# Kernel tuning notes

Hardware: AMD Instinct MI355X
Metric: run time of the kernel (lower is better)

## Reference

```python
import jax, jax.numpy as jnp
import numpy as np

N = 50000        # total nodes (disjoint batch of graphs)
E = 800000       # total edges
F_IN = 8         # node feature dim
S = 6            # edge feature dim
H = 20           # ECC kernel-network hidden size (hidden_states)
N_OUT = 20       # ECC output channels (n_out=hidden_states)
G = 32           # GCN channels
D1 = 16          # first dense
N_GRAPHS = 512   # graphs in batch


def setup_inputs() -> dict:
    key = jax.random.key(0)
    ks = jax.random.split(key, 24)
    r = lambda k, sh, s: jax.random.normal(k, sh, dtype=jnp.float32) * s
    return {
        "x": r(ks[0], (N, F_IN), 1.0),
        "e": r(ks[1], (E, S), 1.0),
        "edge_index": jax.random.randint(ks[2], (2, E), 0, N, dtype=jnp.int32),
        "seg": jnp.sort(jax.random.randint(ks[3], (N,), 0, N_GRAPHS, dtype=jnp.int32)),
        # ECC kernel network: S -> H -> H -> F_IN*N_OUT
        "ecc_w1": r(ks[4], (S, H), 0.4), "ecc_b1": jnp.zeros((H,), jnp.float32),
        "ecc_w2": r(ks[5], (H, H), 0.2), "ecc_b2": jnp.zeros((H,), jnp.float32),
        "ecc_w3": r(ks[6], (H, F_IN * N_OUT), 0.2), "ecc_b3": jnp.zeros((F_IN * N_OUT,), jnp.float32),
        "ecc_root": r(ks[7], (F_IN, N_OUT), 0.3), "ecc_b": jnp.zeros((N_OUT,), jnp.float32),
        "gcn1_w": r(ks[8], (N_OUT, G), 0.2), "gcn1_b": jnp.zeros((G,), jnp.float32),
        "gcn2_w": r(ks[9], (G, G), 0.2), "gcn2_b": jnp.zeros((G,), jnp.float32),
        "d1_w": r(ks[10], (G, D1), 0.2), "d1_b": jnp.zeros((D1,), jnp.float32),
        "d2_w": r(ks[11], (D1, 1), 0.2), "d2_b": jnp.zeros((1,), jnp.float32),
    }


def reference(x, e, edge_index, seg,
              ecc_w1, ecc_b1, ecc_w2, ecc_b2, ecc_w3, ecc_b3, ecc_root, ecc_b,
              gcn1_w, gcn1_b, gcn2_w, gcn2_b, d1_w, d1_b, d2_w, d2_b):
    row, col = edge_index[0], edge_index[1]  # message col -> row

    # --- ECCConv: per-edge MLP produces an [F_IN, N_OUT] filter per edge ---
    h = jax.nn.relu(e @ ecc_w1 + ecc_b1)
    h = jax.nn.relu(h @ ecc_w2 + ecc_b2)
    w_edge = (h @ ecc_w3 + ecc_b3).reshape(E, F_IN, N_OUT)   # [E, F_in, F_out]
    msg = jnp.einsum('ef,efo->eo', x[col], w_edge)            # per-edge message
    agg = jax.ops.segment_sum(msg, row, num_segments=N)
    x1 = jax.nn.relu(agg + x @ ecc_root + ecc_b)              # root + bias + relu

    # --- GCN normalization from the edge list (A + I, symmetric norm) ---
    deg = jax.ops.segment_sum(jnp.ones((E,), x.dtype), row, num_segments=N) + 1.0
    dinv = jax.lax.rsqrt(deg)
    edge_norm = (dinv[row] * dinv[col])[:, None]
    self_norm = (dinv * dinv)[:, None]

    def gcn(hin, W, b):
        hw = hin @ W
        nmsg = jax.ops.segment_sum(edge_norm * hw[col], row, num_segments=N)
        return jax.nn.relu(nmsg + self_norm * hw + b)

    x2 = gcn(x1, gcn1_w, gcn1_b)
    x3 = gcn(x2, gcn2_w, gcn2_b)

    # --- GlobalSumPool over graph ids, then MLP head ---
    pooled = jax.ops.segment_sum(x3, seg, num_segments=N_GRAPHS)  # [n_graphs, G]
    out = (pooled @ d1_w + d1_b) @ d2_w + d2_b                    # [n_graphs, 1]
    return out
```

## Files before the change

kernel.cpp:

```cpp
#include <hip/hip_runtime.h>

#define S_DIM   6
#define H_DIM   20
#define F_INN   8
#define N_OUTC  20
#define G_DIM   32
#define D1_DIM  16
#define NGRAPH  512

typedef short short8 __attribute__((ext_vector_type(8)));
typedef float floatx4 __attribute__((ext_vector_type(4)));

__device__ __forceinline__ unsigned short f2bf(float f) {
    unsigned u = __float_as_uint(f);
    return (unsigned short)((u + 0x8000u) >> 16);
}
__device__ __forceinline__ float bf2f(unsigned short s) {
    return __uint_as_float(((unsigned)s) << 16);
}

__global__ __launch_bounds__(256) void loc_kernel(
    const int* __restrict__ ei, int E, int* __restrict__ cnt,
    int* __restrict__ loc)
{
    int i = blockIdx.x * 256 + threadIdx.x;
    if (i >= E) return;
    loc[i] = atomicAdd(&cnt[ei[i]], 1);
}

__global__ __launch_bounds__(256) void scanA_kernel(
    const int* __restrict__ deg, int N, int* __restrict__ bsum)
{
    int i = blockIdx.x * 256 + threadIdx.x;
    int v = (i < N) ? deg[i] : 0;
#pragma unroll
    for (int d = 1; d < 64; d <<= 1) v += __shfl_down(v, d, 64);
    __shared__ int ws[4];
    int wid = threadIdx.x >> 6;
    if ((threadIdx.x & 63) == 0) ws[wid] = v;
    __syncthreads();
    if (threadIdx.x == 0) bsum[blockIdx.x] = ws[0] + ws[1] + ws[2] + ws[3];
}

__global__ __launch_bounds__(256) void scanC_kernel(
    const int* __restrict__ deg, int N, const int* __restrict__ bsum, int nbl,
    int E, int* __restrict__ rowptr, float* __restrict__ dinv)
{
    __shared__ int ws[4];
    __shared__ int sboff;
    int t = threadIdx.x;
    {
        int v = (t < nbl && t < blockIdx.x) ? bsum[t] : 0;
#pragma unroll
        for (int d = 1; d < 64; d <<= 1) v += __shfl_down(v, d, 64);
        int wid = t >> 6;
        if ((t & 63) == 0) ws[wid] = v;
        __syncthreads();
        if (t == 0) sboff = ws[0] + ws[1] + ws[2] + ws[3];
        __syncthreads();
    }

    int i = blockIdx.x * 256 + t;
    int d0 = (i < N) ? deg[i] : 0;
    int v = d0;
#pragma unroll
    for (int d = 1; d < 64; d <<= 1) {
        int u = __shfl_up(v, d, 64);
        if ((t & 63) >= d) v += u;
    }
    __shared__ int ws2[4];
    int wid = t >> 6;
    if ((t & 63) == 63) ws2[wid] = v;
    __syncthreads();
    int woff = 0;
    for (int w = 0; w < wid; ++w) woff += ws2[w];
    if (i < N) {
        rowptr[i] = sboff + woff + v - d0;
        dinv[i] = rsqrtf((float)d0 + 1.0f);
    }
    if (blockIdx.x == 0 && t == 0) rowptr[N] = E;
}

__global__ __launch_bounds__(256) void build_kernel(
    const int* __restrict__ ei, int E, const int* __restrict__ rowptr,
    const int* __restrict__ loc,
    int* __restrict__ eid_at_slot, int* __restrict__ col_sorted)
{
    int i = blockIdx.x * 256 + threadIdx.x;
    if (i >= E) return;
    int p = rowptr[ei[i]] + loc[i];
    eid_at_slot[p] = i;
    col_sorted[p] = ei[E + i];
}

__global__ __launch_bounds__(256) void ecc_mfma_kernel(
    const float* __restrict__ e, const float* __restrict__ x,
    const int* __restrict__ eid_at_slot, const int* __restrict__ col_sorted,
    const int* __restrict__ rowptr, int N, int E,
    const float* __restrict__ w1, const float* __restrict__ b1,
    const float* __restrict__ w2, const float* __restrict__ b2,
    const float* __restrict__ w3, const float* __restrict__ b3,
    float* __restrict__ agg)
{
    __shared__ char ubuf[256 * N_OUTC * 4];
    __shared__ unsigned short h2b[256][N_OUTC];
    __shared__ unsigned short xb[256][F_INN];
    __shared__ int rbounds[2];

    unsigned short* Bl = (unsigned short*)ubuf;
    float* lmsg = (float*)ubuf;

    int t = threadIdx.x;
    int j0 = blockIdx.x * 256;
    int jend = min(j0 + 256, E);
    int j = j0 + t;

    if (t < 2) {
        int s = (t == 0) ? j0 : (jend - 1);
        int lo = 0, hi = N - 1;
        while (lo < hi) {
            int m = (lo + hi + 1) >> 1;
            if (rowptr[m] <= s) lo = m; else hi = m - 1;
        }
        rbounds[t] = lo;
    }

    for (int idx = t; idx < 6144; idx += 256) {
        int jj   = idx & 7;
        int n    = (idx >> 3) & 15;
        int quad = (idx >> 7) & 3;
        int nt   = (idx >> 9) & 1;
        int s    = idx >> 10;
        int K = 32 * s + quad * 8 + jj;
        int o = n + 16 * nt;
        float v = 0.0f;
        if (o < N_OUTC) {
            if (K < 160)      v = w3[(K >> 3) * 160 + (K & 7) * N_OUTC + o];
            else if (K < 168) v = b3[(K - 160) * N_OUTC + o];
        }
        Bl[idx] = f2bf(v);
    }

    if (j < E) {
        int i = eid_at_slot[j];
        int c = col_sorted[j];

        float ef[S_DIM];
#pragma unroll
        for (int s = 0; s < S_DIM; ++s) ef[s] = e[(size_t)i * S_DIM + s];

        float h1[H_DIM];
#pragma unroll
        for (int jj = 0; jj < H_DIM; ++jj) {
            float a = b1[jj];
#pragma unroll
            for (int s = 0; s < S_DIM; ++s) a = fmaf(ef[s], w1[s * H_DIM + jj], a);
            h1[jj] = fmaxf(a, 0.0f);
        }

        float h2[H_DIM];
#pragma unroll
        for (int jj = 0; jj < H_DIM; ++jj) {
            float a = b2[jj];
#pragma unroll
            for (int k = 0; k < H_DIM; ++k) a = fmaf(h1[k], w2[k * H_DIM + jj], a);
            h2[jj] = fmaxf(a, 0.0f);
        }

        const float4* xp = (const float4*)&x[(size_t)c * F_INN];
        float4 xa = xp[0], xb4 = xp[1];
        float xf[F_INN] = {xa.x, xa.y, xa.z, xa.w, xb4.x, xb4.y, xb4.z, xb4.w};

#pragma unroll
        for (int o = 0; o < N_OUTC; ++o) h2b[t][o] = f2bf(h2[o]);
#pragma unroll
        for (int f = 0; f < F_INN; ++f) xb[t][f] = f2bf(xf[f]);
    } else {
#pragma unroll
        for (int o = 0; o < N_OUTC; ++o) h2b[t][o] = 0;
#pragma unroll
        for (int f = 0; f < F_INN; ++f) xb[t][f] = 0;
    }
    __syncthreads();

    int lane = t & 63;
    int quad = lane >> 4;
    int n = lane & 15;
    short8 Bf[12];
#pragma unroll
    for (int s = 0; s < 6; ++s)
#pragma unroll
        for (int nt = 0; nt < 2; ++nt)
            Bf[s * 2 + nt] = *(const short8*)&Bl[((((s * 2 + nt) * 4 + quad) * 16 + n) * 8)];
    __syncthreads();

    int w = t >> 6;
#pragma unroll
    for (int T = 0; T < 4; ++T) {
        int base = w * 64 + T * 16;
        int m = base + n;

        const short8 xv8 = *(const short8*)&xb[m][0];
        float xfl[F_INN];
#pragma unroll
        for (int jj = 0; jj < F_INN; ++jj) xfl[jj] = bf2f((unsigned short)xv8[jj]);

        floatx4 acc0 = {0.f, 0.f, 0.f, 0.f};
        floatx4 acc1 = {0.f, 0.f, 0.f, 0.f};
#pragma unroll
        for (int s = 0; s < 6; ++s) {
            short8 A = {0, 0, 0, 0, 0, 0, 0, 0};
            if (s < 5) {
                float h = bf2f(h2b[m][4 * s + quad]);
#pragma unroll
                for (int jj = 0; jj < F_INN; ++jj)
                    A[jj] = (short)f2bf(h * xfl[jj]);
            } else if (quad == 0) {
                A = xv8;
            }
            acc0 = __builtin_amdgcn_mfma_f32_16x16x32_bf16(A, Bf[s * 2 + 0], acc0, 0, 0, 0);
            acc1 = __builtin_amdgcn_mfma_f32_16x16x32_bf16(A, Bf[s * 2 + 1], acc1, 0, 0, 0);
        }

#pragma unroll
        for (int r = 0; r < 4; ++r) {
            int row = base + quad * 4 + r;
            lmsg[row * N_OUTC + n] = acc0[r];
            if (n < 4) lmsg[row * N_OUTC + 16 + n] = acc1[r];
        }
    }
    __syncthreads();

    int r0 = rbounds[0], r1 = rbounds[1];
    int work = (r1 - r0 + 1) * 5;
    for (int ww = t; ww < work; ww += 256) {
        int row = r0 + ww / 5;
        int q = ww - (ww / 5) * 5;
        int a0 = rowptr[row], a1 = rowptr[row + 1];
        int s0 = max(a0, j0), s1 = min(a1, jend);
        float4 acc = make_float4(0.f, 0.f, 0.f, 0.f);
        for (int s = s0; s < s1; ++s) {
            const float4 v = *(const float4*)&lmsg[(s - j0) * N_OUTC + q * 4];
            acc.x += v.x; acc.y += v.y; acc.z += v.z; acc.w += v.w;
        }
        float* dst = &agg[(size_t)row * N_OUTC + q * 4];
        if (a0 >= j0 && a1 <= jend) {
            *(float4*)dst = acc;
        } else {
            unsafeAtomicAdd(dst + 0, acc.x);
            unsafeAtomicAdd(dst + 1, acc.y);
            unsafeAtomicAdd(dst + 2, acc.z);
            unsafeAtomicAdd(dst + 3, acc.w);
        }
    }
}

__global__ __launch_bounds__(256) void node1_kernel(
    const float* __restrict__ agg, const float* __restrict__ x,
    const float* __restrict__ dinv, int N,
    const float* __restrict__ root, const float* __restrict__ eb,
    const float* __restrict__ g1w,
    float* __restrict__ hws1)
{
    int n = blockIdx.x * 256 + threadIdx.x;
    if (n >= N) return;

    const float4* xp = (const float4*)&x[(size_t)n * F_INN];
    float4 xa = xp[0], xb = xp[1];
    float xf[F_INN] = {xa.x, xa.y, xa.z, xa.w, xb.x, xb.y, xb.z, xb.w};

    float x1[N_OUTC];
#pragma unroll
    for (int o = 0; o < N_OUTC; ++o) {
        float a = agg[(size_t)n * N_OUTC + o] + eb[o];
#pragma unroll
        for (int f = 0; f < F_INN; ++f) a = fmaf(xf[f], root[f * N_OUTC + o], a);
        x1[o] = fmaxf(a, 0.0f);
    }

    float di = dinv[n];
    float4* hp = (float4*)&hws1[(size_t)n * G_DIM];
#pragma unroll
    for (int q = 0; q < G_DIM / 4; ++q) {
        float4 v;
        float* vv = &v.x;
#pragma unroll
        for (int u = 0; u < 4; ++u) {
            int g = q * 4 + u;
            float a = 0.0f;
#pragma unroll
            for (int o = 0; o < N_OUTC; ++o) a = fmaf(x1[o], g1w[o * G_DIM + g], a);
            vv[u] = a * di;
        }
        hp[q] = v;
    }
}

template<bool DO_MATMUL>
__global__ __launch_bounds__(256) void gcn_gather_kernel(
    const float* __restrict__ hws, const int* __restrict__ rowptr,
    const int* __restrict__ col_sorted, const float* __restrict__ dinv, int N,
    const float* __restrict__ bias, const float* __restrict__ w2,
    float* __restrict__ outbuf)
{
    __shared__ float x2s[32 * 33];
    __shared__ float w2s[G_DIM * G_DIM];

    int t = threadIdx.x;
    int nl = t >> 3;
    int q = t & 7;
    int n = blockIdx.x * 32 + nl;

    if (DO_MATMUL) {
        ((float4*)w2s)[t] = ((const float4*)w2)[t];
    }

    float4 xo = make_float4(0.f, 0.f, 0.f, 0.f);
    float di = 0.0f;
    if (n < N) {
        di = dinv[n];
        int j0 = rowptr[n], j1 = rowptr[n + 1];
        float4 s = *(const float4*)&hws[(size_t)n * G_DIM + q * 4];
        for (int j = j0; j < j1; ++j) {
            int c = col_sorted[j];
            float4 v = *(const float4*)&hws[(size_t)c * G_DIM + q * 4];
            s.x += v.x; s.y += v.y; s.z += v.z; s.w += v.w;
        }
        const float4 b4 = *(const float4*)&bias[q * 4];
        xo.x = fmaxf(fmaf(di, s.x, b4.x), 0.0f);
        xo.y = fmaxf(fmaf(di, s.y, b4.y), 0.0f);
        xo.z = fmaxf(fmaf(di, s.z, b4.z), 0.0f);
        xo.w = fmaxf(fmaf(di, s.w, b4.w), 0.0f);
    }

    if (DO_MATMUL) {
        x2s[nl * 33 + q * 4 + 0] = xo.x;
        x2s[nl * 33 + q * 4 + 1] = xo.y;
        x2s[nl * 33 + q * 4 + 2] = xo.z;
        x2s[nl * 33 + q * 4 + 3] = xo.w;
        __syncthreads();
        if (n < N) {
            float a0 = 0.f, a1 = 0.f, a2 = 0.f, a3 = 0.f;
            const float* xr = &x2s[nl * 33];
#pragma unroll
            for (int g = 0; g < G_DIM; ++g) {
                float xv = xr[g];
                a0 = fmaf(xv, w2s[g * G_DIM + q * 4 + 0], a0);
                a1 = fmaf(xv, w2s[g * G_DIM + q * 4 + 1], a1);
                a2 = fmaf(xv, w2s[g * G_DIM + q * 4 + 2], a2);
                a3 = fmaf(xv, w2s[g * G_DIM + q * 4 + 3], a3);
            }
            *(float4*)&outbuf[(size_t)n * G_DIM + q * 4] =
                make_float4(a0 * di, a1 * di, a2 * di, a3 * di);
        }
    } else {
        if (n < N)
            *(float4*)&outbuf[(size_t)n * G_DIM + q * 4] = xo;
    }
}

__global__ __launch_bounds__(256) void pool_head_kernel(
    const float* __restrict__ x3, const int* __restrict__ seg, int N,
    const float* __restrict__ d1w, const float* __restrict__ d1b,
    const float* __restrict__ d2w, const float* __restrict__ d2b,
    float* __restrict__ out)
{
    __shared__ float red[8][G_DIM];
    __shared__ float pvec[G_DIM];
    __shared__ int bounds[2];
    int g = blockIdx.x;
    int t = threadIdx.x;
    if (t < 2) {
        int target = g + t;
        int lo = 0, hi = N;
        while (lo < hi) {
            int m = (lo + hi) >> 1;
            if (seg[m] < target) lo = m + 1; else hi = m;
        }
        bounds[t] = lo;
    }
    __syncthreads();
    int n0 = bounds[0], n1 = bounds[1];
    int ch = t & (G_DIM - 1);
    int slice = t >> 5;
    float a = 0.0f;
    for (int n = n0 + slice; n < n1; n += 8)
        a += x3[(size_t)n * G_DIM + ch];
    red[slice][ch] = a;
    __syncthreads();
    if (slice == 0) {
        float s = red[0][ch];
#pragma unroll
        for (int k = 1; k < 8; ++k) s += red[k][ch];
        pvec[ch] = s;
    }
    __syncthreads();
    if (t < 64) {
        float acc = 0.0f;
        if (t < D1_DIM) {
            float tj = d1b[t];
#pragma unroll
            for (int gg = 0; gg < G_DIM; ++gg)
                tj = fmaf(pvec[gg], d1w[gg * D1_DIM + t], tj);
            acc = tj * d2w[t];
        }
#pragma unroll
        for (int d = 1; d < D1_DIM; d <<= 1) acc += __shfl_down(acc, d, 64);
        if (t == 0) out[g] = acc + d2b[0];
    }
}

extern "C" void kernel_launch(void* const* d_in, const int* in_sizes, int n_in,
                              void* d_out, int out_size, void* d_ws, size_t ws_size,
                              hipStream_t stream)
{
    const float* x    = (const float*)d_in[0];
    const float* e    = (const float*)d_in[1];
    const int*   ei   = (const int*)d_in[2];
    const int*   seg  = (const int*)d_in[3];
    const float* w1   = (const float*)d_in[4];
    const float* b1   = (const float*)d_in[5];
    const float* w2   = (const float*)d_in[6];
    const float* b2   = (const float*)d_in[7];
    const float* w3   = (const float*)d_in[8];
    const float* b3   = (const float*)d_in[9];
    const float* root = (const float*)d_in[10];
    const float* eb   = (const float*)d_in[11];
    const float* g1w  = (const float*)d_in[12];
    const float* g1b  = (const float*)d_in[13];
    const float* g2w  = (const float*)d_in[14];
    const float* g2b  = (const float*)d_in[15];
    const float* d1w  = (const float*)d_in[16];
    const float* d1b  = (const float*)d_in[17];
    const float* d2w  = (const float*)d_in[18];
    const float* d2b  = (const float*)d_in[19];

    const int N = in_sizes[3];
    const int E = in_sizes[1] / S_DIM;
    float* out = (float*)d_out;

    const int nbl = (N + 255) / 256;
    const int ebl = (E + 255) / 256;

    char* ws = (char*)d_ws;
    size_t off = 0;
    auto alloc = [&](size_t elems) -> char* {
        char* p = ws + off;
        off += ((elems * 4 + 15) & ~(size_t)15);
        return p;
    };
    int*   cnt        = (int*)  alloc(N);
    float* agg        = (float*)alloc((size_t)N * N_OUTC);
    size_t zero_bytes = off;
    int*   rowptr     = (int*)  alloc(N + 1);
    int*   bsum       = (int*)  alloc(nbl);
    float* dinv       = (float*)alloc(N);
    int*   loc        = (int*)  alloc(E);
    int*   eid_at_slot= (int*)  alloc(E);
    int*   col_sorted = (int*)  alloc(E);
    float* hws1       = (float*)alloc((size_t)N * G_DIM);
    float* hws2       = (float*)alloc((size_t)N * G_DIM);
    float* x3         = (float*)alloc((size_t)N * G_DIM);
    (void)ws_size;

    hipMemsetAsync(d_ws, 0, zero_bytes, stream);

    loc_kernel<<<ebl, 256, 0, stream>>>(ei, E, cnt, loc);
    scanA_kernel<<<nbl, 256, 0, stream>>>(cnt, N, bsum);
    scanC_kernel<<<nbl, 256, 0, stream>>>(cnt, N, bsum, nbl, E, rowptr, dinv);
    build_kernel<<<ebl, 256, 0, stream>>>(ei, E, rowptr, loc, eid_at_slot, col_sorted);
    ecc_mfma_kernel<<<ebl, 256, 0, stream>>>(e, x, eid_at_slot, col_sorted,
                                             rowptr, N, E,
                                             w1, b1, w2, b2, w3, b3, agg);
    node1_kernel<<<nbl, 256, 0, stream>>>(agg, x, dinv, N, root, eb, g1w, hws1);
    gcn_gather_kernel<true><<<(N + 31) / 32, 256, 0, stream>>>(
        hws1, rowptr, col_sorted, dinv, N, g1b, g2w, hws2);
    gcn_gather_kernel<false><<<(N + 31) / 32, 256, 0, stream>>>(
        hws2, rowptr, col_sorted, dinv, N, g2b, nullptr, x3);
    pool_head_kernel<<<NGRAPH, 256, 0, stream>>>(x3, seg, N, d1w, d1b, d2w, d2b, out);
}
```

Baseline: 306.8 us.

## Store GCN node features in bf16 and shrink ECC kernel shared memory

The intermediate node feature buffers (hws1, hws2, x3) move from fp32 to bf16, halving the bytes read in the random-neighbour gathers of both GCN layers and in pooling. The gather kernels now have each thread handle 8 channels with 16-byte loads, covering 64 nodes per block. Separately, the ECC kernel overlaps its message buffer with the B-fragment, h2 and x staging areas in one smaller shared array, keeping MFMA accumulators in registers until a barrier. This lowers LDS use for higher occupancy, at the cost of bf16 rounding error in the GCN activations and more register pressure.

```diff
diff --git a/kernel.cpp b/kernel.cpp
--- a/kernel.cpp
+++ b/kernel.cpp
@@ -102,13 +102,12 @@
     const float* __restrict__ w3, const float* __restrict__ b3,
     float* __restrict__ agg)
 {
-    __shared__ char ubuf[256 * N_OUTC * 4];
-    __shared__ unsigned short h2b[256][N_OUTC];
-    __shared__ unsigned short xb[256][F_INN];
+    __shared__ char smem[26624];
     __shared__ int rbounds[2];
-
-    unsigned short* Bl = (unsigned short*)ubuf;
-    float* lmsg = (float*)ubuf;
+    unsigned short* Bl = (unsigned short*)smem;
+    unsigned short (*h2b)[N_OUTC] = (unsigned short (*)[N_OUTC])(smem + 12288);
+    unsigned short (*xb)[F_INN]   = (unsigned short (*)[F_INN])(smem + 22528);
+    float* lmsg = (float*)smem;
 
     int t = threadIdx.x;
     int j0 = blockIdx.x * 256;
@@ -192,9 +191,9 @@
 #pragma unroll
         for (int nt = 0; nt < 2; ++nt)
             Bf[s * 2 + nt] = *(const short8*)&Bl[((((s * 2 + nt) * 4 + quad) * 16 + n) * 8)];
-    __syncthreads();
 
     int w = t >> 6;
+    floatx4 acc0s[4], acc1s[4];
 #pragma unroll
     for (int T = 0; T < 4; ++T) {
         int base = w * 64 + T * 16;
@@ -221,12 +220,19 @@
             acc0 = __builtin_amdgcn_mfma_f32_16x16x32_bf16(A, Bf[s * 2 + 0], acc0, 0, 0, 0);
             acc1 = __builtin_amdgcn_mfma_f32_16x16x32_bf16(A, Bf[s * 2 + 1], acc1, 0, 0, 0);
         }
-
+        acc0s[T] = acc0;
+        acc1s[T] = acc1;
+    }
+    __syncthreads();
+
+#pragma unroll
+    for (int T = 0; T < 4; ++T) {
+        int base = w * 64 + T * 16;
 #pragma unroll
         for (int r = 0; r < 4; ++r) {
             int row = base + quad * 4 + r;
-            lmsg[row * N_OUTC + n] = acc0[r];
-            if (n < 4) lmsg[row * N_OUTC + 16 + n] = acc1[r];
+            lmsg[row * N_OUTC + n] = acc0s[T][r];
+            if (n < 4) lmsg[row * N_OUTC + 16 + n] = acc1s[T][r];
         }
     }
     __syncthreads();
@@ -260,7 +266,7 @@
     const float* __restrict__ dinv, int N,
     const float* __restrict__ root, const float* __restrict__ eb,
     const float* __restrict__ g1w,
-    float* __restrict__ hws1)
+    unsigned short* __restrict__ hws1)
 {
     int n = blockIdx.x * 256 + threadIdx.x;
     if (n >= N) return;
@@ -279,88 +285,95 @@
     }
 
     float di = dinv[n];
-    float4* hp = (float4*)&hws1[(size_t)n * G_DIM];
-#pragma unroll
-    for (int q = 0; q < G_DIM / 4; ++q) {
-        float4 v;
-        float* vv = &v.x;
-#pragma unroll
-        for (int u = 0; u < 4; ++u) {
-            int g = q * 4 + u;
+#pragma unroll
+    for (int q = 0; q < 4; ++q) {
+        short8 o8;
+#pragma unroll
+        for (int u = 0; u < 8; ++u) {
+            int g = q * 8 + u;
             float a = 0.0f;
 #pragma unroll
             for (int o = 0; o < N_OUTC; ++o) a = fmaf(x1[o], g1w[o * G_DIM + g], a);
-            vv[u] = a * di;
-        }
-        hp[q] = v;
+            o8[u] = (short)f2bf(a * di);
+        }
+        *(short8*)&hws1[(size_t)n * G_DIM + q * 8] = o8;
     }
 }
 
 template<bool DO_MATMUL>
 __global__ __launch_bounds__(256) void gcn_gather_kernel(
-    const float* __restrict__ hws, const int* __restrict__ rowptr,
+    const unsigned short* __restrict__ hws, const int* __restrict__ rowptr,
     const int* __restrict__ col_sorted, const float* __restrict__ dinv, int N,
     const float* __restrict__ bias, const float* __restrict__ w2,
-    float* __restrict__ outbuf)
-{
-    __shared__ float x2s[32 * 33];
+    unsigned short* __restrict__ outbuf)
+{
+    __shared__ float x2s[64][33];
     __shared__ float w2s[G_DIM * G_DIM];
 
     int t = threadIdx.x;
-    int nl = t >> 3;
-    int q = t & 7;
-    int n = blockIdx.x * 32 + nl;
+    int nl = t >> 2;
+    int q = t & 3;
+    int n = blockIdx.x * 64 + nl;
 
     if (DO_MATMUL) {
         ((float4*)w2s)[t] = ((const float4*)w2)[t];
     }
 
-    float4 xo = make_float4(0.f, 0.f, 0.f, 0.f);
+    float xo[8];
     float di = 0.0f;
     if (n < N) {
         di = dinv[n];
         int j0 = rowptr[n], j1 = rowptr[n + 1];
-        float4 s = *(const float4*)&hws[(size_t)n * G_DIM + q * 4];
+        short8 sv = *(const short8*)&hws[(size_t)n * G_DIM + q * 8];
+        float s[8];
+#pragma unroll
+        for (int k = 0; k < 8; ++k) s[k] = bf2f((unsigned short)sv[k]);
         for (int j = j0; j < j1; ++j) {
             int c = col_sorted[j];
-            float4 v = *(const float4*)&hws[(size_t)c * G_DIM + q * 4];
-            s.x += v.x; s.y += v.y; s.z += v.z; s.w += v.w;
-        }
-        const float4 b4 = *(const float4*)&bias[q * 4];
-        xo.x = fmaxf(fmaf(di, s.x, b4.x), 0.0f);
-        xo.y = fmaxf(fmaf(di, s.y, b4.y), 0.0f);
-        xo.z = fmaxf(fmaf(di, s.z, b4.z), 0.0f);
-        xo.w = fmaxf(fmaf(di, s.w, b4.w), 0.0f);
+            short8 v = *(const short8*)&hws[(size_t)c * G_DIM + q * 8];
+#pragma unroll
+            for (int k = 0; k < 8; ++k) s[k] += bf2f((unsigned short)v[k]);
+        }
+#pragma unroll
+        for (int k = 0; k < 8; ++k)
+            xo[k] = fmaxf(fmaf(di, s[k], bias[q * 8 + k]), 0.0f);
+    } else {
+#pragma unroll
+        for (int k = 0; k < 8; ++k) xo[k] = 0.0f;
     }
 
     if (DO_MATMUL) {
-        x2s[nl * 33 + q * 4 + 0] = xo.x;
-        x2s[nl * 33 + q * 4 + 1] = xo.y;
-        x2s[nl * 33 + q * 4 + 2] = xo.z;
-        x2s[nl * 33 + q * 4 + 3] = xo.w;
+#pragma unroll
+        for (int k = 0; k < 8; ++k) x2s[nl][q * 8 + k] = xo[k];
         __syncthreads();
         if (n < N) {
-            float a0 = 0.f, a1 = 0.f, a2 = 0.f, a3 = 0.f;
-            const float* xr = &x2s[nl * 33];
+            float a[8];
+#pragma unroll
+            for (int k = 0; k < 8; ++k) a[k] = 0.0f;
 #pragma unroll
             for (int g = 0; g < G_DIM; ++g) {
-                float xv = xr[g];
-                a0 = fmaf(xv, w2s[g * G_DIM + q * 4 + 0], a0);
-                a1 = fmaf(xv, w2s[g * G_DIM + q * 4 + 1], a1);
-                a2 = fmaf(xv, w2s[g * G_DIM + q * 4 + 2], a2);
-                a3 = fmaf(xv, w2s[g * G_DIM + q * 4 + 3], a3);
+                float xv = x2s[nl][g];
+#pragma unroll
+                for (int k = 0; k < 8; ++k)
+                    a[k] = fmaf(xv, w2s[g * G_DIM + q * 8 + k], a[k]);
             }
-            *(float4*)&outbuf[(size_t)n * G_DIM + q * 4] =
-                make_float4(a0 * di, a1 * di, a2 * di, a3 * di);
+            short8 o8;
+#pragma unroll
+            for (int k = 0; k < 8; ++k) o8[k] = (short)f2bf(a[k] * di);
+            *(short8*)&outbuf[(size_t)n * G_DIM + q * 8] = o8;
         }
     } else {
-        if (n < N)
-            *(float4*)&outbuf[(size_t)n * G_DIM + q * 4] = xo;
+        if (n < N) {
+            short8 o8;
+#pragma unroll
+            for (int k = 0; k < 8; ++k) o8[k] = (short)f2bf(xo[k]);
+            *(short8*)&outbuf[(size_t)n * G_DIM + q * 8] = o8;
+        }
     }
 }
 
 __global__ __launch_bounds__(256) void pool_head_kernel(
-    const float* __restrict__ x3, const int* __restrict__ seg, int N,
+    const unsigned short* __restrict__ x3, const int* __restrict__ seg, int N,
     const float* __restrict__ d1w, const float* __restrict__ d1b,
     const float* __restrict__ d2w, const float* __restrict__ d2b,
     float* __restrict__ out)
@@ -385,7 +398,7 @@
     int slice = t >> 5;
     float a = 0.0f;
     for (int n = n0 + slice; n < n1; n += 8)
-        a += x3[(size_t)n * G_DIM + ch];
+        a += bf2f(x3[(size_t)n * G_DIM + ch]);
     red[slice][ch] = a;
     __syncthreads();
     if (slice == 0) {
@@ -458,9 +471,9 @@
     int*   loc        = (int*)  alloc(E);
     int*   eid_at_slot= (int*)  alloc(E);
     int*   col_sorted = (int*)  alloc(E);
-    float* hws1       = (float*)alloc((size_t)N * G_DIM);
-    float* hws2       = (float*)alloc((size_t)N * G_DIM);
-    float* x3         = (float*)alloc((size_t)N * G_DIM);
+    unsigned short* hws1 = (unsigned short*)alloc((size_t)N * G_DIM / 2);
+    unsigned short* hws2 = (unsigned short*)alloc((size_t)N * G_DIM / 2);
+    unsigned short* x3   = (unsigned short*)alloc((size_t)N * G_DIM / 2);
     (void)ws_size;
 
     hipMemsetAsync(d_ws, 0, zero_bytes, stream);
@@ -473,9 +486,9 @@
                                              rowptr, N, E,
                                              w1, b1, w2, b2, w3, b3, agg);
     node1_kernel<<<nbl, 256, 0, stream>>>(agg, x, dinv, N, root, eb, g1w, hws1);
-    gcn_gather_kernel<true><<<(N + 31) / 32, 256, 0, stream>>>(
+    gcn_gather_kernel<true><<<(N + 63) / 64, 256, 0, stream>>>(
         hws1, rowptr, col_sorted, dinv, N, g1b, g2w, hws2);
-    gcn_gather_kernel<false><<<(N + 31) / 32, 256, 0, stream>>>(
+    gcn_gather_kernel<false><<<(N + 63) / 64, 256, 0, stream>>>(
         hws2, rowptr, col_sorted, dinv, N, g2b, nullptr, x3);
     pool_head_kernel<<<NGRAPH, 256, 0, stream>>>(x3, seg, N, d1w, d1b, d2w, d2b, out);
 }
```

Measured after the change: 292.2 us. -4.8%, faster.
